# Kernel tuning notes

Hardware: AMD Instinct MI355X
Metric: run time of the kernel (lower is better)

Reference implementation:

```python
import jax, jax.numpy as jnp
import numpy as np
import math

IN_C, OUT_C, NUM_PARAM, STRIDE = 128, 256, 9, 1
BN_EPS = 1e-5


def _make_p_n(num_param):
    base_int = round(math.sqrt(num_param))
    row_number = num_param // base_int
    mod_number = num_param % base_int
    gx, gy = np.meshgrid(np.arange(row_number), np.arange(base_int), indexing='ij')
    px, py = gx.flatten(), gy.flatten()
    if mod_number > 0:
        mx, my = np.meshgrid(np.arange(row_number, row_number + 1), np.arange(mod_number), indexing='ij')
        px = np.concatenate([px, mx.flatten()])
        py = np.concatenate([py, my.flatten()])
    return np.concatenate([px, py]).astype(np.float32)  # (2N,)


def setup_inputs() -> dict:
    key = jax.random.key(0)
    ks = jax.random.split(key, 8)
    x = jax.random.normal(ks[0], (8, IN_C, 80, 80), dtype=jnp.float32)
    # offset-predicting conv (torch inits this to 0; use small random weights to exercise gathers)
    w_pconv = jax.random.normal(ks[1], (2 * NUM_PARAM, IN_C, 3, 3), dtype=jnp.float32) * 0.01
    b_pconv = jax.random.normal(ks[2], (2 * NUM_PARAM,), dtype=jnp.float32) * 0.1
    # final Conv: kernel (num_param, 1), stride (num_param, 1), pad 0, no bias
    w_conv = jax.random.normal(ks[3], (OUT_C, IN_C, NUM_PARAM, 1), dtype=jnp.float32) * (1.0 / math.sqrt(IN_C * NUM_PARAM))
    bn_gamma = jnp.ones((OUT_C,), jnp.float32) + 0.1 * jax.random.normal(ks[4], (OUT_C,), jnp.float32)
    bn_beta = 0.1 * jax.random.normal(ks[5], (OUT_C,), jnp.float32)
    bn_mean = 0.1 * jax.random.normal(ks[6], (OUT_C,), jnp.float32)
    bn_var = jnp.abs(jax.random.normal(ks[7], (OUT_C,), jnp.float32)) + 0.5
    p_n = jnp.asarray(_make_p_n(NUM_PARAM))
    return {"x": x, "w_pconv": w_pconv, "b_pconv": b_pconv, "w_conv": w_conv,
            "bn_gamma": bn_gamma, "bn_beta": bn_beta, "bn_mean": bn_mean,
            "bn_var": bn_var, "p_n": p_n}


def _conv2d(x, w, strides, padding):
    return jax.lax.conv_general_dilated(x, w, window_strides=strides, padding=padding,
                                        dimension_numbers=('NCHW', 'OIHW', 'NCHW'))


def reference(x, w_pconv, b_pconv, w_conv, bn_gamma, bn_beta, bn_mean, bn_var, p_n):
    b, c, H, W = x.shape
    # per-pixel offsets: [b, 2N, h, w]
    offset = _conv2d(x, w_pconv, (STRIDE, STRIDE), 'SAME') + b_pconv[None, :, None, None]
    N = offset.shape[1] // 2
    h, w = offset.shape[2], offset.shape[3]

    # sampling locations p = p_0 + p_n + offset
    px0 = jnp.broadcast_to((jnp.arange(h, dtype=x.dtype) * STRIDE)[None, None, :, None], (1, N, h, w))
    py0 = jnp.broadcast_to((jnp.arange(w, dtype=x.dtype) * STRIDE)[None, None, None, :], (1, N, h, w))
    p0 = jnp.concatenate([px0, py0], axis=1)  # [1, 2N, h, w]
    p = (p0 + p_n[None, :, None, None] + offset).transpose(0, 2, 3, 1)  # [b, h, w, 2N]

    def clamp2(t):
        return jnp.concatenate([jnp.clip(t[..., :N], 0, H - 1), jnp.clip(t[..., N:], 0, W - 1)], axis=-1)

    q_lt = clamp2(jnp.floor(p)).astype(jnp.int32)
    q_rb = clamp2(jnp.floor(p) + 1).astype(jnp.int32)
    q_lb = jnp.concatenate([q_lt[..., :N], q_rb[..., N:]], axis=-1)
    q_rt = jnp.concatenate([q_rb[..., :N], q_lt[..., N:]], axis=-1)
    pc = clamp2(p)

    # bilinear weights [b, h, w, N]
    def g(q, sx, sy):
        qf = q.astype(pc.dtype)
        return (1 + sx * (qf[..., :N] - pc[..., :N])) * (1 + sy * (qf[..., N:] - pc[..., N:]))

    g_lt, g_rb = g(q_lt, 1.0, 1.0), g(q_rb, -1.0, -1.0)
    g_lb, g_rt = g(q_lb, 1.0, -1.0), g(q_rt, -1.0, 1.0)

    x_flat = x.reshape(b, c, H * W)

    def gather(q):
        idx = (q[..., :N] * W + q[..., N:]).reshape(b, -1)  # [b, h*w*N]
        out = jax.vmap(lambda xf, i: xf[:, i])(x_flat, idx)  # [b, c, h*w*N]
        return out.reshape(b, c, h, w, N)

    x_off = (g_lt[:, None] * gather(q_lt) + g_rb[:, None] * gather(q_rb)
             + g_lb[:, None] * gather(q_lb) + g_rt[:, None] * gather(q_rt))

    # b c h w n -> b c (h n) w
    x_off = x_off.transpose(0, 1, 2, 4, 3).reshape(b, c, h * N, w)

    y = _conv2d(x_off, w_conv, (N, 1), 'VALID')  # [b, out_c, h, w]
    inv = jax.lax.rsqrt(bn_var + BN_EPS)
    y = (y - bn_mean[None, :, None, None]) * (bn_gamma * inv)[None, :, None, None] + bn_beta[None, :, None, None]
    return y * jax.nn.sigmoid(y)  # SiLU
```

## Files before the change

### kernel.cpp

```cpp
#include <hip/hip_runtime.h>
#include <hip/hip_bf16.h>


typedef __attribute__((ext_vector_type(8))) short bf16x8;
typedef __attribute__((ext_vector_type(4))) float f32x4;
typedef __attribute__((ext_vector_type(2))) float f32x2;
typedef __attribute__((ext_vector_type(4))) unsigned int u32x4;

#define NHW 6400
#define NPIX 80

__device__ __forceinline__ unsigned short f2bf(float f){
  __hip_bfloat16 h = __float2bfloat16(f);
  unsigned short u; __builtin_memcpy(&u, &h, 2); return u;
}
__device__ __forceinline__ f32x2 bfp2f(unsigned int u){
  union { unsigned int i; float f; } a, b;
  a.i = u << 16; b.i = u & 0xffff0000u;
  f32x2 r; r.x = a.f; r.y = b.f; return r;
}
__device__ __forceinline__ unsigned pk_bf16(float a, float b){
  unsigned r;
  asm("v_cvt_pk_bf16_f32 %0, %1, %2" : "=v"(r) : "v"(a), "v"(b));
  return r;
}
__device__ __forceinline__ void splitbf(float v, unsigned short& hi, unsigned short& lo){
  hi = f2bf(v);
  union { unsigned int i; float f; } h; h.i = (unsigned)hi << 16;
  lo = f2bf(v - h.f);
}
__device__ __forceinline__ float f16u2f(unsigned int u){
  unsigned short s = (unsigned short)u; _Float16 h;
  __builtin_memcpy(&h, &s, 2); return (float)h;
}
__device__ __forceinline__ unsigned short f2f16u(float f){
  _Float16 h = (_Float16)f; unsigned short s;
  __builtin_memcpy(&s, &h, 2); return s;
}
__device__ __forceinline__ float fast_silu(float v){
  float e, r;
  asm("v_exp_f32 %0, %1" : "=v"(e) : "v"(v * -1.44269504088896f));
  asm("v_rcp_f32 %0, %1" : "=v"(r) : "v"(1.0f + e));
  return v * r;
}

__global__ __launch_bounds__(256) void k_pre(const float* __restrict__ x,
                                             const float* __restrict__ w_conv,
                                             const float* __restrict__ w_pconv,
                                             const float* __restrict__ gamma,
                                             const float* __restrict__ beta,
                                             const float* __restrict__ mean,
                                             const float* __restrict__ var,
                                             unsigned short* __restrict__ xt,
                                             unsigned short* __restrict__ xtl,
                                             uint4* __restrict__ wf,
                                             uint4* __restrict__ wpfH,
                                             uint4* __restrict__ wpfL,
                                             float* __restrict__ shift){
  __shared__ unsigned short tileH[64 * 132];
  __shared__ unsigned short tileL[64 * 132];
  int blk = blockIdx.x; int t = threadIdx.x;
  if (blk < 800){
    int b = blk / 100; int pixbase = (blk % 100) * 64;
    int lane = t & 63; int cg = t >> 6;
    for (int ci = 0; ci < 32; ++ci){
      int c = cg * 32 + ci;
      float v = x[(b * 128 + c) * NHW + pixbase + lane];
      unsigned short hi, lo; splitbf(v, hi, lo);
      tileH[lane * 132 + c] = hi;
      tileL[lane * 132 + c] = lo;
    }
    __syncthreads();
    for (int i = 0; i < 8; ++i){
      int slot = t + i * 256; int m = slot >> 5; int c = (slot & 31) * 4;
      uint2 vH = *reinterpret_cast<const uint2*>(&tileH[m * 132 + c]);
      uint2 vL = *reinterpret_cast<const uint2*>(&tileL[m * 132 + c]);
      *reinterpret_cast<uint2*>(xt  + (b * NHW + pixbase + m) * 128 + c) = vH;
      *reinterpret_cast<uint2*>(xtl + (b * NHW + pixbase + m) * 128 + c) = vL;
    }
    return;
  }
  int pblk = blk - 800;
  if (pblk < 144){
    int id = pblk * 256 + t;
    int lane = id & 63, ofrag = (id >> 6) & 15, kc = (id >> 10) & 3, n = id >> 12;
    int o = ofrag * 16 + (lane & 15), cb = kc * 32 + ((lane >> 4) & 3) * 8;
    float sc = gamma[o] * rsqrtf(var[o] + 1e-5f);
    unsigned short h[8];
    for (int j = 0; j < 8; ++j) h[j] = f2bf(w_conv[(o * 128 + cb + j) * 9 + n] * sc);
    uint4 v;
    v.x = (unsigned)h[0] | ((unsigned)h[1] << 16);
    v.y = (unsigned)h[2] | ((unsigned)h[3] << 16);
    v.z = (unsigned)h[4] | ((unsigned)h[5] << 16);
    v.w = (unsigned)h[6] | ((unsigned)h[7] << 16);
    wf[id] = v;
  } else if (pblk < 180){
    int isLo = (pblk >= 162);
    int id = (pblk - (isLo ? 162 : 144)) * 256 + t;
    int lane = id & 63, ofrag = (id >> 6) & 1, kc = (id >> 7) & 3, tap = id >> 9;
    int o = ofrag * 16 + (lane & 15), cb = kc * 32 + ((lane >> 4) & 3) * 8;
    unsigned short h[8];
    for (int j = 0; j < 8; ++j){
      unsigned short hi = 0, lo = 0;
      if (o < 18) splitbf(w_pconv[(o * 128 + cb + j) * 9 + tap], hi, lo);
      h[j] = isLo ? lo : hi;
    }
    uint4 v;
    v.x = (unsigned)h[0] | ((unsigned)h[1] << 16);
    v.y = (unsigned)h[2] | ((unsigned)h[3] << 16);
    v.z = (unsigned)h[4] | ((unsigned)h[5] << 16);
    v.w = (unsigned)h[6] | ((unsigned)h[7] << 16);
    if (isLo) wpfL[id] = v; else wpfH[id] = v;
  } else {
    float sc = gamma[t] * rsqrtf(var[t] + 1e-5f);
    shift[t] = beta[t] - mean[t] * sc;
  }
}

__global__ __launch_bounds__(256, 6) void k_offconv(const unsigned short* __restrict__ xt,
                                                    const unsigned short* __restrict__ xtl,
                                                    const uint4* __restrict__ wpfH,
                                                    const uint4* __restrict__ wpfL,
                                                    const float* __restrict__ bpc,
                                                    const float* __restrict__ pn,
                                                    uint4* __restrict__ desc){
  int bid = blockIdx.x;
  int blk = (bid & 7) * 200 + (bid >> 3);
  int b = blk / 200; int pixbase = (blk % 200) * 32;
  int t = threadIdx.x; int lane = t & 63; int wv = t >> 6;
  int og = wv & 1;
  int pf = wv >> 1;
  __shared__ short BtileH[32 * 136];
  __shared__ short BtileL[32 * 136];
  __shared__ float off_lds[32 * 20];

  f32x4 acc = (f32x4){0.f, 0.f, 0.f, 0.f};
  const unsigned short* xbH = xt  + (size_t)b * NHW * 128;
  const unsigned short* xbL = xtl + (size_t)b * NHW * 128;

  int m_i[4], c_i[4], h_i[4], w_i[4];
#pragma unroll
  for (int i = 0; i < 4; ++i){
    int slot = t + i * 256;
    m_i[i] = slot >> 5; c_i[i] = (slot & 31) * 4;
    int p = pixbase + m_i[i];
    h_i[i] = p / NPIX; w_i[i] = p % NPIX;
  }

  uint2 rH[4], rL[4];

#define LOADTAP(DH, DW)                                                        \
  _Pragma("unroll")                                                            \
  for (int i = 0; i < 4; ++i){                                                 \
    int h2 = h_i[i] + (DH), w2 = w_i[i] + (DW);                                \
    uint2 vH; vH.x = 0u; vH.y = 0u;                                            \
    uint2 vL; vL.x = 0u; vL.y = 0u;                                            \
    if ((unsigned)h2 < NPIX && (unsigned)w2 < NPIX){                           \
      int off = (h2 * NPIX + w2) * 128 + c_i[i];                               \
      vH = *reinterpret_cast<const uint2*>(xbH + off);                         \
      vL = *reinterpret_cast<const uint2*>(xbL + off);                         \
    }                                                                          \
    rH[i] = vH; rL[i] = vL;                                                    \
  }

#define WRITETILE()                                                            \
  _Pragma("unroll")                                                            \
  for (int i = 0; i < 4; ++i){                                                 \
    *reinterpret_cast<uint2*>(&BtileH[m_i[i] * 136 + c_i[i]]) = rH[i];         \
    *reinterpret_cast<uint2*>(&BtileL[m_i[i] * 136 + c_i[i]]) = rL[i];         \
  }

  LOADTAP(-1, -1)
  WRITETILE()
  __syncthreads();

#pragma unroll 1
  for (int tap = 0; tap < 9; ++tap){
    if (tap < 8){
      int dh2 = (tap + 1) / 3 - 1, dw2 = (tap + 1) % 3 - 1;
      LOADTAP(dh2, dw2)
    }
#pragma unroll
    for (int kc = 0; kc < 4; ++kc){
      int boff = (pf * 16 + (lane & 15)) * 136 + kc * 32 + ((lane >> 4) & 3) * 8;
      bf16x8 bH = *reinterpret_cast<const bf16x8*>(&BtileH[boff]);
      bf16x8 bL = *reinterpret_cast<const bf16x8*>(&BtileL[boff]);
      int widx = ((tap * 4 + kc) * 2 + og) * 64 + lane;
      bf16x8 aH = *reinterpret_cast<const bf16x8*>(&wpfH[widx]);
      bf16x8 aL = *reinterpret_cast<const bf16x8*>(&wpfL[widx]);
      acc = __builtin_amdgcn_mfma_f32_16x16x32_bf16(aH, bH, acc, 0, 0, 0);
      acc = __builtin_amdgcn_mfma_f32_16x16x32_bf16(aH, bL, acc, 0, 0, 0);
      acc = __builtin_amdgcn_mfma_f32_16x16x32_bf16(aL, bH, acc, 0, 0, 0);
      acc = __builtin_amdgcn_mfma_f32_16x16x32_bf16(aL, bL, acc, 0, 0, 0);
    }
    __syncthreads();
    if (tap < 8){
      WRITETILE()
      __syncthreads();
    }
  }

  int pl = pf * 16 + (lane & 15);
#pragma unroll
  for (int r = 0; r < 4; ++r){
    int o = og * 16 + ((lane >> 4) & 3) * 4 + r;
    if (o < 18) off_lds[pl * 20 + o] = acc[r] + bpc[o];
  }
  __syncthreads();

  for (int item = t; item < 288; item += 256){
    int m = item / 9, n = item % 9;
    int p = pixbase + m; int h = p / NPIX, w = p % NPIX;
    float px = (float)h + pn[n]     + off_lds[m * 20 + n];
    float py = (float)w + pn[9 + n] + off_lds[m * 20 + 9 + n];
    float flx = floorf(px), fly = floorf(py);
    float qltx = fminf(fmaxf(flx, 0.f), 79.f);
    float qrbx = fminf(fmaxf(flx + 1.f, 0.f), 79.f);
    float qlty = fminf(fmaxf(fly, 0.f), 79.f);
    float qrby = fminf(fmaxf(fly + 1.f, 0.f), 79.f);
    float pcx = fminf(fmaxf(px, 0.f), 79.f);
    float pcy = fminf(fmaxf(py, 0.f), 79.f);
    float dxl = 1.f + (qltx - pcx), dxr = 1.f - (qrbx - pcx);
    float dyl = 1.f + (qlty - pcy), dyr = 1.f - (qrby - pcy);
    unsigned ix_l = (unsigned)(int)qltx, ix_r = (unsigned)(int)qrbx;
    unsigned iy_l = (unsigned)(int)qlty, iy_r = (unsigned)(int)qrby;
    uint4 d;
    d.x = (ix_l * NPIX + iy_l) | ((ix_r * NPIX + iy_r) << 16);
    d.y = (ix_l * NPIX + iy_r) | ((ix_r * NPIX + iy_l) << 16);
    d.z = (unsigned)f2f16u(dxl * dyl) | ((unsigned)f2f16u(dxr * dyr) << 16);
    d.w = (unsigned)f2f16u(dxl * dyr) | ((unsigned)f2f16u(dxr * dyl) << 16);
    desc[(size_t)(b * 9 + n) * NHW + p] = d;
  }
#undef LOADTAP
#undef WRITETILE
}

__global__ __launch_bounds__(256, 4) void k_main(const unsigned short* __restrict__ xt,
                                                 const uint4* __restrict__ desc,
                                                 const uint4* __restrict__ wf,
                                                 const float* __restrict__ shift,
                                                 float* __restrict__ out){
  int bid = blockIdx.x;
  int blk = (bid & 7) * 200 + (bid >> 3);
  int b = blk / 200; int pixbase = (blk % 200) * 32;
  int t = threadIdx.x; int lane = t & 63; int ow = t >> 6;
  __shared__ alignas(16) char A_lds[2][32 * 256];

  const char* xb = (const char*)(xt + (size_t)b * NHW * 128);
  const uint4* descb = desc + (size_t)b * 9 * NHW + pixbase;

  int m0 = t >> 4;
  int m1 = m0 + 16;
  int cb = (t & 15) * 16;
  int ls0 = m0 * 256 + (cb ^ ((m0 & 7) << 4));
  int ls1 = m1 * 256 + (cb ^ ((m1 & 7) << 4));

  f32x4 acc[4][2];
#pragma unroll
  for (int of = 0; of < 4; ++of)
#pragma unroll
    for (int pf = 0; pf < 2; ++pf)
      acc[of][pf] = (f32x4){0.f, 0.f, 0.f, 0.f};

  u32x4 GX[4], GY[4];
  uint2 zwX, zwY;
  uint4 dB0, dB1;

#define ISSUE_X()                                                              \
  {                                                                            \
    zwX.x = dB0.z; zwX.y = dB0.w;                                              \
    GX[0] = *reinterpret_cast<const u32x4*>(xb + (dB0.x & 0xffffu) * 256u + (unsigned)cb); \
    GX[1] = *reinterpret_cast<const u32x4*>(xb + (dB0.x >> 16)     * 256u + (unsigned)cb); \
    GX[2] = *reinterpret_cast<const u32x4*>(xb + (dB0.y & 0xffffu) * 256u + (unsigned)cb); \
    GX[3] = *reinterpret_cast<const u32x4*>(xb + (dB0.y >> 16)     * 256u + (unsigned)cb); \
  }

#define ISSUE_Y()                                                              \
  {                                                                            \
    zwY.x = dB1.z; zwY.y = dB1.w;                                              \
    GY[0] = *reinterpret_cast<const u32x4*>(xb + (dB1.x & 0xffffu) * 256u + (unsigned)cb); \
    GY[1] = *reinterpret_cast<const u32x4*>(xb + (dB1.x >> 16)     * 256u + (unsigned)cb); \
    GY[2] = *reinterpret_cast<const u32x4*>(xb + (dB1.y & 0xffffu) * 256u + (unsigned)cb); \
    GY[3] = *reinterpret_cast<const u32x4*>(xb + (dB1.y >> 16)     * 256u + (unsigned)cb); \
  }

#define COMB(G, ZW, LSO, WB)                                                   \
  {                                                                            \
    float w0 = f16u2f(ZW.x & 0xffffu), w1 = f16u2f(ZW.x >> 16);                \
    float w2 = f16u2f(ZW.y & 0xffffu), w3 = f16u2f(ZW.y >> 16);                \
    u32x4 pk;                                                                  \
    _Pragma("unroll")                                                          \
    for (int j = 0; j < 4; ++j){                                               \
      f32x2 a = w0 * bfp2f(G[0][j]) + w1 * bfp2f(G[1][j])                      \
              + w2 * bfp2f(G[2][j]) + w3 * bfp2f(G[3][j]);                     \
      pk[j] = pk_bf16(a.x, a.y);                                               \
    }                                                                          \
    *reinterpret_cast<u32x4*>((WB) + (LSO)) = pk;                              \
  }

#define MFMA_HALF(NN, KCA, KCB)                                                \
  {                                                                            \
    const char* ab = &A_lds[(NN) & 1][0];                                      \
    __builtin_amdgcn_s_setprio(1);                                             \
    _Pragma("unroll")                                                          \
    for (int kc = (KCA); kc <= (KCB); ++kc){                                   \
      bf16x8 bfrk[2];                                                          \
      _Pragma("unroll")                                                        \
      for (int pf = 0; pf < 2; ++pf){                                          \
        int row = pf * 16 + (lane & 15);                                       \
        bfrk[pf] = *reinterpret_cast<const bf16x8*>(                           \
            ab + row * 256 + ((kc * 64 + ((lane >> 4) & 3) * 16) ^ ((row & 7) << 4))); \
      }                                                                        \
      _Pragma("unroll")                                                        \
      for (int of = 0; of < 4; ++of){                                          \
        bf16x8 afr = *reinterpret_cast<const bf16x8*>(                         \
            &wf[((((NN) * 4 + kc) * 16) + ow * 4 + of) * 64 + lane]);          \
        _Pragma("unroll")                                                      \
        for (int pf = 0; pf < 2; ++pf)                                         \
          acc[of][pf] = __builtin_amdgcn_mfma_f32_16x16x32_bf16(afr, bfrk[pf], acc[of][pf], 0, 0, 0); \
      }                                                                        \
    }                                                                          \
    __builtin_amdgcn_s_setprio(0);                                             \
  }

#define STEP(NN)                                                               \
  {                                                                            \
    if ((NN) < 8){ ISSUE_X() }                                                 \
    if ((NN) < 7){ dB0 = descb[(size_t)((NN) + 2) * NHW + m0]; }               \
    MFMA_HALF(NN, 0, 1)                                                        \
    if ((NN) < 8){                                                             \
      COMB(GX, zwX, ls0, &A_lds[((NN) + 1) & 1][0])                            \
      __builtin_amdgcn_sched_barrier(0);                                       \
      ISSUE_Y()                                                                \
    }                                                                          \
    if ((NN) < 7){ dB1 = descb[(size_t)((NN) + 2) * NHW + m1]; }               \
    MFMA_HALF(NN, 2, 3)                                                        \
    if ((NN) < 8){                                                             \
      COMB(GY, zwY, ls1, &A_lds[((NN) + 1) & 1][0])                            \
    }                                                                          \
    __syncthreads();                                                           \
  }

  dB0 = descb[m0]; dB1 = descb[m1];
  ISSUE_X()
  COMB(GX, zwX, ls0, &A_lds[0][0])
  __builtin_amdgcn_sched_barrier(0);
  ISSUE_Y()
  COMB(GY, zwY, ls1, &A_lds[0][0])
  dB0 = descb[NHW + m0]; dB1 = descb[NHW + m1];
  __syncthreads();

  STEP(0) STEP(1) STEP(2) STEP(3) STEP(4) STEP(5) STEP(6) STEP(7) STEP(8)

#pragma unroll
  for (int of = 0; of < 4; ++of)
#pragma unroll
    for (int pf = 0; pf < 2; ++pf){
      int pix = pixbase + pf * 16 + (lane & 15);
#pragma unroll
      for (int r = 0; r < 4; ++r){
        int o = ow * 64 + of * 16 + ((lane >> 4) & 3) * 4 + r;
        float v = acc[of][pf][r] + shift[o];
        out[(size_t)(b * 256 + o) * NHW + pix] = fast_silu(v);
      }
    }
#undef ISSUE_X
#undef ISSUE_Y
#undef COMB
#undef MFMA_HALF
#undef STEP
}

extern "C" void kernel_launch(void* const* d_in, const int* in_sizes, int n_in,
                              void* d_out, int out_size, void* d_ws, size_t ws_size,
                              hipStream_t stream){
  const float* x       = (const float*)d_in[0];
  const float* w_pconv = (const float*)d_in[1];
  const float* b_pconv = (const float*)d_in[2];
  const float* w_conv  = (const float*)d_in[3];
  const float* gamma   = (const float*)d_in[4];
  const float* beta    = (const float*)d_in[5];
  const float* mean    = (const float*)d_in[6];
  const float* var     = (const float*)d_in[7];
  const float* pn      = (const float*)d_in[8];

  char* ws = (char*)d_ws;
  unsigned short* xt  = (unsigned short*)(ws + 0);
  unsigned short* xtl = (unsigned short*)(ws + 13107200);
  uint4* desc         = (uint4*)(ws + 26214400);
  uint4* wf           = (uint4*)(ws + 33587200);
  uint4* wpfH         = (uint4*)(ws + 34177024);
  uint4* wpfL         = (uint4*)(ws + 34250752);
  float* shift        = (float*)(ws + 34324480);
  float* out          = (float*)d_out;

  k_pre<<<981, 256, 0, stream>>>(x, w_conv, w_pconv, gamma, beta, mean, var,
                                 xt, xtl, wf, wpfH, wpfL, shift);
  k_offconv<<<1600, 256, 0, stream>>>(xt, xtl, wpfH, wpfL, b_pconv, pn, desc);
  k_main<<<1600, 256, 0, stream>>>(xt, desc, wf, shift, out);
}
```

Baseline: 116.7 us.

## Prefetch MFMA weight fragments into registers one step ahead and reorder gather pipeline

Weight fragments for the MFMA were loaded from global memory inline inside the MFMA loop. They are now prefetched into register arrays (Wa, Wb) during the previous step, so the MFMA loop reads only registers. The gather issue, combine and descriptor loads are reordered with sched_barriers: the X gathers are issued before the first MFMA half and combined after it, and the Y gathers follow the same pattern around the second half. This is meant to hide global-load latency behind matrix work, at the cost of 16 extra bf16x8 registers per thread, which may reduce occupancy.

```diff
diff --git a/kernel.cpp b/kernel.cpp
--- a/kernel.cpp
+++ b/kernel.cpp
@@ -263,12 +263,11 @@
       acc[of][pf] = (f32x4){0.f, 0.f, 0.f, 0.f};
 
   u32x4 GX[4], GY[4];
-  uint2 zwX, zwY;
   uint4 dB0, dB1;
+  bf16x8 Wa[8], Wb[8];
 
 #define ISSUE_X()                                                              \
   {                                                                            \
-    zwX.x = dB0.z; zwX.y = dB0.w;                                              \
     GX[0] = *reinterpret_cast<const u32x4*>(xb + (dB0.x & 0xffffu) * 256u + (unsigned)cb); \
     GX[1] = *reinterpret_cast<const u32x4*>(xb + (dB0.x >> 16)     * 256u + (unsigned)cb); \
     GX[2] = *reinterpret_cast<const u32x4*>(xb + (dB0.y & 0xffffu) * 256u + (unsigned)cb); \
@@ -277,17 +276,16 @@
 
 #define ISSUE_Y()                                                              \
   {                                                                            \
-    zwY.x = dB1.z; zwY.y = dB1.w;                                              \
     GY[0] = *reinterpret_cast<const u32x4*>(xb + (dB1.x & 0xffffu) * 256u + (unsigned)cb); \
     GY[1] = *reinterpret_cast<const u32x4*>(xb + (dB1.x >> 16)     * 256u + (unsigned)cb); \
     GY[2] = *reinterpret_cast<const u32x4*>(xb + (dB1.y & 0xffffu) * 256u + (unsigned)cb); \
     GY[3] = *reinterpret_cast<const u32x4*>(xb + (dB1.y >> 16)     * 256u + (unsigned)cb); \
   }
 
-#define COMB(G, ZW, LSO, WB)                                                   \
-  {                                                                            \
-    float w0 = f16u2f(ZW.x & 0xffffu), w1 = f16u2f(ZW.x >> 16);                \
-    float w2 = f16u2f(ZW.y & 0xffffu), w3 = f16u2f(ZW.y >> 16);                \
+#define COMB(G, D, LSO, WB)                                                    \
+  {                                                                            \
+    float w0 = f16u2f(D.z & 0xffffu), w1 = f16u2f(D.z >> 16);                  \
+    float w2 = f16u2f(D.w & 0xffffu), w3 = f16u2f(D.w >> 16);                  \
     u32x4 pk;                                                                  \
     _Pragma("unroll")                                                          \
     for (int j = 0; j < 4; ++j){                                               \
@@ -298,7 +296,17 @@
     *reinterpret_cast<u32x4*>((WB) + (LSO)) = pk;                              \
   }
 
-#define MFMA_HALF(NN, KCA, KCB)                                                \
+#define WLOAD(W, NN, KCA)                                                      \
+  {                                                                            \
+    _Pragma("unroll")                                                          \
+    for (int j = 0; j < 8; ++j){                                               \
+      int kc = (KCA) + (j >> 2); int of = j & 3;                               \
+      W[j] = *reinterpret_cast<const bf16x8*>(                                 \
+          &wf[((((NN) * 4 + kc) * 16) + ow * 4 + of) * 64 + lane]);            \
+    }                                                                          \
+  }
+
+#define MFMA_HALF(NN, KCA, KCB, W)                                             \
   {                                                                            \
     const char* ab = &A_lds[(NN) & 1][0];                                      \
     __builtin_amdgcn_s_setprio(1);                                             \
@@ -313,8 +321,7 @@
       }                                                                        \
       _Pragma("unroll")                                                        \
       for (int of = 0; of < 4; ++of){                                          \
-        bf16x8 afr = *reinterpret_cast<const bf16x8*>(                         \
-            &wf[((((NN) * 4 + kc) * 16) + ow * 4 + of) * 64 + lane]);          \
+        bf16x8 afr = W[(kc - (KCA)) * 4 + of];                                 \
         _Pragma("unroll")                                                      \
         for (int pf = 0; pf < 2; ++pf)                                         \
           acc[of][pf] = __builtin_amdgcn_mfma_f32_16x16x32_bf16(afr, bfrk[pf], acc[of][pf], 0, 0, 0); \
@@ -326,28 +333,37 @@
 #define STEP(NN)                                                               \
   {                                                                            \
     if ((NN) < 8){ ISSUE_X() }                                                 \
+    __builtin_amdgcn_sched_barrier(0);                                         \
+    MFMA_HALF(NN, 0, 1, Wa)                                                    \
+    if ((NN) < 8){                                                             \
+      WLOAD(Wa, (NN) + 1, 0)                                                   \
+      __builtin_amdgcn_sched_barrier(0);                                       \
+      COMB(GX, dB0, ls0, &A_lds[((NN) + 1) & 1][0])                            \
+    }                                                                          \
     if ((NN) < 7){ dB0 = descb[(size_t)((NN) + 2) * NHW + m0]; }               \
-    MFMA_HALF(NN, 0, 1)                                                        \
+    __builtin_amdgcn_sched_barrier(0);                                         \
+    if ((NN) < 8){ ISSUE_Y() }                                                 \
+    __builtin_amdgcn_sched_barrier(0);                                         \
+    MFMA_HALF(NN, 2, 3, Wb)                                                    \
     if ((NN) < 8){                                                             \
-      COMB(GX, zwX, ls0, &A_lds[((NN) + 1) & 1][0])                            \
+      WLOAD(Wb, (NN) + 1, 2)                                                   \
       __builtin_amdgcn_sched_barrier(0);                                       \
-      ISSUE_Y()                                                                \
+      COMB(GY, dB1, ls1, &A_lds[((NN) + 1) & 1][0])                            \
     }                                                                          \
     if ((NN) < 7){ dB1 = descb[(size_t)((NN) + 2) * NHW + m1]; }               \
-    MFMA_HALF(NN, 2, 3)                                                        \
-    if ((NN) < 8){                                                             \
-      COMB(GY, zwY, ls1, &A_lds[((NN) + 1) & 1][0])                            \
-    }                                                                          \
     __syncthreads();                                                           \
   }
 
   dB0 = descb[m0]; dB1 = descb[m1];
   ISSUE_X()
-  COMB(GX, zwX, ls0, &A_lds[0][0])
+  WLOAD(Wa, 0, 0)
+  WLOAD(Wb, 0, 2)
+  COMB(GX, dB0, ls0, &A_lds[0][0])
+  dB0 = descb[NHW + m0];
   __builtin_amdgcn_sched_barrier(0);
   ISSUE_Y()
-  COMB(GY, zwY, ls1, &A_lds[0][0])
-  dB0 = descb[NHW + m0]; dB1 = descb[NHW + m1];
+  COMB(GY, dB1, ls1, &A_lds[0][0])
+  dB1 = descb[NHW + m1];
   __syncthreads();
 
   STEP(0) STEP(1) STEP(2) STEP(3) STEP(4) STEP(5) STEP(6) STEP(7) STEP(8)
@@ -367,6 +383,7 @@
 #undef ISSUE_X
 #undef ISSUE_Y
 #undef COMB
+#undef WLOAD
 #undef MFMA_HALF
 #undef STEP
 }
```

Measured after the change: 167.4 us. 1.43x slower.

## Fuse offset conv and deformable gather-GEMM into one kernel via LDS descriptors

Applied to the files above, without the earlier changes.

Merges the offset-predicting conv kernel and the main gather/GEMM kernel into a single kernel with the same block-to-pixel mapping. Per-block sampling descriptors now stay in shared memory instead of a global round trip, which also removes one launch. Shared memory is aliased between the offset-conv tiles and the main A buffers. The cost is lower occupancy for the offset-conv phase (launch bounds 4 instead of 6) and serialisation of both phases within each block.

```diff
diff --git a/kernel.cpp b/kernel.cpp
--- a/kernel.cpp
+++ b/kernel.cpp
@@ -117,37 +117,42 @@
   }
 }
 
-__global__ __launch_bounds__(256, 6) void k_offconv(const unsigned short* __restrict__ xt,
-                                                    const unsigned short* __restrict__ xtl,
-                                                    const uint4* __restrict__ wpfH,
-                                                    const uint4* __restrict__ wpfL,
-                                                    const float* __restrict__ bpc,
-                                                    const float* __restrict__ pn,
-                                                    uint4* __restrict__ desc){
+__global__ __launch_bounds__(256, 4) void k_fused(const unsigned short* __restrict__ xt,
+                                                  const unsigned short* __restrict__ xtl,
+                                                  const uint4* __restrict__ wpfH,
+                                                  const uint4* __restrict__ wpfL,
+                                                  const float* __restrict__ bpc,
+                                                  const float* __restrict__ pn,
+                                                  const uint4* __restrict__ wf,
+                                                  const float* __restrict__ shift,
+                                                  float* __restrict__ out){
   int bid = blockIdx.x;
   int blk = (bid & 7) * 200 + (bid >> 3);
   int b = blk / 200; int pixbase = (blk % 200) * 32;
-  int t = threadIdx.x; int lane = t & 63; int wv = t >> 6;
-  int og = wv & 1;
-  int pf = wv >> 1;
-  __shared__ short BtileH[32 * 136];
-  __shared__ short BtileL[32 * 136];
-  __shared__ float off_lds[32 * 20];
-
-  f32x4 acc = (f32x4){0.f, 0.f, 0.f, 0.f};
-  const unsigned short* xbH = xt  + (size_t)b * NHW * 128;
-  const unsigned short* xbL = xtl + (size_t)b * NHW * 128;
-
-  int m_i[4], c_i[4], h_i[4], w_i[4];
-#pragma unroll
-  for (int i = 0; i < 4; ++i){
-    int slot = t + i * 256;
-    m_i[i] = slot >> 5; c_i[i] = (slot & 31) * 4;
-    int p = pixbase + m_i[i];
-    h_i[i] = p / NPIX; w_i[i] = p % NPIX;
-  }
-
-  uint2 rH[4], rL[4];
+  int t = threadIdx.x; int lane = t & 63;
+
+  __shared__ alignas(16) char smem[24576];
+  short* BtileH  = (short*)(smem);
+  short* BtileL  = (short*)(smem + 8704);
+  float* off_lds = (float*)(smem + 17408);
+  uint4* descL   = (uint4*)(smem + 19968);
+
+  {
+    int wv = t >> 6; int og = wv & 1; int pf = wv >> 1;
+    f32x4 acc = (f32x4){0.f, 0.f, 0.f, 0.f};
+    const unsigned short* xbH = xt  + (size_t)b * NHW * 128;
+    const unsigned short* xbL = xtl + (size_t)b * NHW * 128;
+
+    int m_i[4], c_i[4], h_i[4], w_i[4];
+#pragma unroll
+    for (int i = 0; i < 4; ++i){
+      int slot = t + i * 256;
+      m_i[i] = slot >> 5; c_i[i] = (slot & 31) * 4;
+      int p = pixbase + m_i[i];
+      h_i[i] = p / NPIX; w_i[i] = p % NPIX;
+    }
+
+    uint2 rH[4], rL[4];
 
 #define LOADTAP(DH, DW)                                                        \
   _Pragma("unroll")                                                            \
@@ -170,101 +175,96 @@
     *reinterpret_cast<uint2*>(&BtileL[m_i[i] * 136 + c_i[i]]) = rL[i];         \
   }
 
-  LOADTAP(-1, -1)
-  WRITETILE()
-  __syncthreads();
+    LOADTAP(-1, -1)
+    WRITETILE()
+    __syncthreads();
 
 #pragma unroll 1
-  for (int tap = 0; tap < 9; ++tap){
-    if (tap < 8){
-      int dh2 = (tap + 1) / 3 - 1, dw2 = (tap + 1) % 3 - 1;
-      LOADTAP(dh2, dw2)
-    }
-#pragma unroll
-    for (int kc = 0; kc < 4; ++kc){
-      int boff = (pf * 16 + (lane & 15)) * 136 + kc * 32 + ((lane >> 4) & 3) * 8;
-      bf16x8 bH = *reinterpret_cast<const bf16x8*>(&BtileH[boff]);
-      bf16x8 bL = *reinterpret_cast<const bf16x8*>(&BtileL[boff]);
-      int widx = ((tap * 4 + kc) * 2 + og) * 64 + lane;
-      bf16x8 aH = *reinterpret_cast<const bf16x8*>(&wpfH[widx]);
-      bf16x8 aL = *reinterpret_cast<const bf16x8*>(&wpfL[widx]);
-      acc = __builtin_amdgcn_mfma_f32_16x16x32_bf16(aH, bH, acc, 0, 0, 0);
-      acc = __builtin_amdgcn_mfma_f32_16x16x32_bf16(aH, bL, acc, 0, 0, 0);
-      acc = __builtin_amdgcn_mfma_f32_16x16x32_bf16(aL, bH, acc, 0, 0, 0);
-      acc = __builtin_amdgcn_mfma_f32_16x16x32_bf16(aL, bL, acc, 0, 0, 0);
+    for (int tap = 0; tap < 9; ++tap){
+      if (tap < 8){
+        int dh2 = (tap + 1) / 3 - 1, dw2 = (tap + 1) % 3 - 1;
+        LOADTAP(dh2, dw2)
+      }
+#pragma unroll
+      for (int kc = 0; kc < 4; ++kc){
+        int boff = (pf * 16 + (lane & 15)) * 136 + kc * 32 + ((lane >> 4) & 3) * 8;
+        bf16x8 bH = *reinterpret_cast<const bf16x8*>(&BtileH[boff]);
+        bf16x8 bL = *reinterpret_cast<const bf16x8*>(&BtileL[boff]);
+        int widx = ((tap * 4 + kc) * 2 + og) * 64 + lane;
+        bf16x8 aH = *reinterpret_cast<const bf16x8*>(&wpfH[widx]);
+        bf16x8 aL = *reinterpret_cast<const bf16x8*>(&wpfL[widx]);
+        acc = __builtin_amdgcn_mfma_f32_16x16x32_bf16(aH, bH, acc, 0, 0, 0);
+        acc = __builtin_amdgcn_mfma_f32_16x16x32_bf16(aH, bL, acc, 0, 0, 0);
+        acc = __builtin_amdgcn_mfma_f32_16x16x32_bf16(aL, bH, acc, 0, 0, 0);
+        acc = __builtin_amdgcn_mfma_f32_16x16x32_bf16(aL, bL, acc, 0, 0, 0);
+      }
+      __syncthreads();
+      if (tap < 8){
+        WRITETILE()
+        __syncthreads();
+      }
+    }
+
+    int pl = pf * 16 + (lane & 15);
+#pragma unroll
+    for (int r = 0; r < 4; ++r){
+      int o = og * 16 + ((lane >> 4) & 3) * 4 + r;
+      if (o < 18) off_lds[pl * 20 + o] = acc[r] + bpc[o];
     }
     __syncthreads();
-    if (tap < 8){
-      WRITETILE()
-      __syncthreads();
-    }
-  }
-
-  int pl = pf * 16 + (lane & 15);
-#pragma unroll
-  for (int r = 0; r < 4; ++r){
-    int o = og * 16 + ((lane >> 4) & 3) * 4 + r;
-    if (o < 18) off_lds[pl * 20 + o] = acc[r] + bpc[o];
-  }
-  __syncthreads();
-
-  for (int item = t; item < 288; item += 256){
-    int m = item / 9, n = item % 9;
-    int p = pixbase + m; int h = p / NPIX, w = p % NPIX;
-    float px = (float)h + pn[n]     + off_lds[m * 20 + n];
-    float py = (float)w + pn[9 + n] + off_lds[m * 20 + 9 + n];
-    float flx = floorf(px), fly = floorf(py);
-    float qltx = fminf(fmaxf(flx, 0.f), 79.f);
-    float qrbx = fminf(fmaxf(flx + 1.f, 0.f), 79.f);
-    float qlty = fminf(fmaxf(fly, 0.f), 79.f);
-    float qrby = fminf(fmaxf(fly + 1.f, 0.f), 79.f);
-    float pcx = fminf(fmaxf(px, 0.f), 79.f);
-    float pcy = fminf(fmaxf(py, 0.f), 79.f);
-    float dxl = 1.f + (qltx - pcx), dxr = 1.f - (qrbx - pcx);
-    float dyl = 1.f + (qlty - pcy), dyr = 1.f - (qrby - pcy);
-    unsigned ix_l = (unsigned)(int)qltx, ix_r = (unsigned)(int)qrbx;
-    unsigned iy_l = (unsigned)(int)qlty, iy_r = (unsigned)(int)qrby;
-    uint4 d;
-    d.x = (ix_l * NPIX + iy_l) | ((ix_r * NPIX + iy_r) << 16);
-    d.y = (ix_l * NPIX + iy_r) | ((ix_r * NPIX + iy_l) << 16);
-    d.z = (unsigned)f2f16u(dxl * dyl) | ((unsigned)f2f16u(dxr * dyr) << 16);
-    d.w = (unsigned)f2f16u(dxl * dyr) | ((unsigned)f2f16u(dxr * dyl) << 16);
-    desc[(size_t)(b * 9 + n) * NHW + p] = d;
-  }
+
+    for (int item = t; item < 288; item += 256){
+      int m = item / 9, n = item % 9;
+      int p = pixbase + m; int h = p / NPIX, w = p % NPIX;
+      float px = (float)h + pn[n]     + off_lds[m * 20 + n];
+      float py = (float)w + pn[9 + n] + off_lds[m * 20 + 9 + n];
+      float flx = floorf(px), fly = floorf(py);
+      float qltx = fminf(fmaxf(flx, 0.f), 79.f);
+      float qrbx = fminf(fmaxf(flx + 1.f, 0.f), 79.f);
+      float qlty = fminf(fmaxf(fly, 0.f), 79.f);
+      float qrby = fminf(fmaxf(fly + 1.f, 0.f), 79.f);
+      float pcx = fminf(fmaxf(px, 0.f), 79.f);
+      float pcy = fminf(fmaxf(py, 0.f), 79.f);
+      float dxl = 1.f + (qltx - pcx), dxr = 1.f - (qrbx - pcx);
+      float dyl = 1.f + (qlty - pcy), dyr = 1.f - (qrby - pcy);
+      unsigned ix_l = (unsigned)(int)qltx, ix_r = (unsigned)(int)qrbx;
+      unsigned iy_l = (unsigned)(int)qlty, iy_r = (unsigned)(int)qrby;
+      uint4 d;
+      d.x = (ix_l * NPIX + iy_l) | ((ix_r * NPIX + iy_r) << 16);
+      d.y = (ix_l * NPIX + iy_r) | ((ix_r * NPIX + iy_l) << 16);
+      d.z = (unsigned)f2f16u(dxl * dyl) | ((unsigned)f2f16u(dxr * dyr) << 16);
+      d.w = (unsigned)f2f16u(dxl * dyr) | ((unsigned)f2f16u(dxr * dyl) << 16);
+      descL[n * 32 + m] = d;
+    }
 #undef LOADTAP
 #undef WRITETILE
-}
-
-__global__ __launch_bounds__(256, 4) void k_main(const unsigned short* __restrict__ xt,
-                                                 const uint4* __restrict__ desc,
-                                                 const uint4* __restrict__ wf,
-                                                 const float* __restrict__ shift,
-                                                 float* __restrict__ out){
-  int bid = blockIdx.x;
-  int blk = (bid & 7) * 200 + (bid >> 3);
-  int b = blk / 200; int pixbase = (blk % 200) * 32;
-  int t = threadIdx.x; int lane = t & 63; int ow = t >> 6;
-  __shared__ alignas(16) char A_lds[2][32 * 256];
-
-  const char* xb = (const char*)(xt + (size_t)b * NHW * 128);
-  const uint4* descb = desc + (size_t)b * 9 * NHW + pixbase;
-
-  int m0 = t >> 4;
-  int m1 = m0 + 16;
-  int cb = (t & 15) * 16;
-  int ls0 = m0 * 256 + (cb ^ ((m0 & 7) << 4));
-  int ls1 = m1 * 256 + (cb ^ ((m1 & 7) << 4));
-
-  f32x4 acc[4][2];
-#pragma unroll
-  for (int of = 0; of < 4; ++of)
-#pragma unroll
-    for (int pf = 0; pf < 2; ++pf)
-      acc[of][pf] = (f32x4){0.f, 0.f, 0.f, 0.f};
-
-  u32x4 GX[4], GY[4];
-  uint2 zwX, zwY;
-  uint4 dB0, dB1;
+  }
+  __syncthreads();
+  __builtin_amdgcn_sched_barrier(0);
+
+  {
+    int ow = t >> 6;
+    char* A_lds0 = smem;
+    const char* xb = (const char*)(xt + (size_t)b * NHW * 128);
+
+    int m0 = t >> 4;
+    int m1 = m0 + 16;
+    int cb = (t & 15) * 16;
+    int ls0 = m0 * 256 + (cb ^ ((m0 & 7) << 4));
+    int ls1 = m1 * 256 + (cb ^ ((m1 & 7) << 4));
+
+    f32x4 acc[4][2];
+#pragma unroll
+    for (int of = 0; of < 4; ++of)
+#pragma unroll
+      for (int pf = 0; pf < 2; ++pf)
+        acc[of][pf] = (f32x4){0.f, 0.f, 0.f, 0.f};
+
+    u32x4 GX[4], GY[4];
+    uint2 zwX, zwY;
+    uint4 dB0, dB1;
+
+#define DLD(N, M) descL[(N) * 32 + (M)]
 
 #define ISSUE_X()                                                              \
   {                                                                            \
@@ -300,7 +300,7 @@
 
 #define MFMA_HALF(NN, KCA, KCB)                                                \
   {                                                                            \
-    const char* ab = &A_lds[(NN) & 1][0];                                      \
+    const char* ab = A_lds0 + ((NN) & 1) * 8192;                               \
     __builtin_amdgcn_s_setprio(1);                                             \
     _Pragma("unroll")                                                          \
     for (int kc = (KCA); kc <= (KCB); ++kc){                                   \
@@ -326,49 +326,51 @@
 #define STEP(NN)                                                               \
   {                                                                            \
     if ((NN) < 8){ ISSUE_X() }                                                 \
-    if ((NN) < 7){ dB0 = descb[(size_t)((NN) + 2) * NHW + m0]; }               \
+    if ((NN) < 7){ dB0 = DLD((NN) + 2, m0); }                                  \
     MFMA_HALF(NN, 0, 1)                                                        \
     if ((NN) < 8){                                                             \
-      COMB(GX, zwX, ls0, &A_lds[((NN) + 1) & 1][0])                            \
+      COMB(GX, zwX, ls0, A_lds0 + (((NN) + 1) & 1) * 8192)                     \
       __builtin_amdgcn_sched_barrier(0);                                       \
       ISSUE_Y()                                                                \
     }                                                                          \
-    if ((NN) < 7){ dB1 = descb[(size_t)((NN) + 2) * NHW + m1]; }               \
+    if ((NN) < 7){ dB1 = DLD((NN) + 2, m1); }                                  \
     MFMA_HALF(NN, 2, 3)                                                        \
     if ((NN) < 8){                                                             \
-      COMB(GY, zwY, ls1, &A_lds[((NN) + 1) & 1][0])                            \
+      COMB(GY, zwY, ls1, A_lds0 + (((NN) + 1) & 1) * 8192)                     \
     }                                                                          \
     __syncthreads();                                                           \
   }
 
-  dB0 = descb[m0]; dB1 = descb[m1];
-  ISSUE_X()
-  COMB(GX, zwX, ls0, &A_lds[0][0])
-  __builtin_amdgcn_sched_barrier(0);
-  ISSUE_Y()
-  COMB(GY, zwY, ls1, &A_lds[0][0])
-  dB0 = descb[NHW + m0]; dB1 = descb[NHW + m1];
-  __syncthreads();
-
-  STEP(0) STEP(1) STEP(2) STEP(3) STEP(4) STEP(5) STEP(6) STEP(7) STEP(8)
-
-#pragma unroll
-  for (int of = 0; of < 4; ++of)
-#pragma unroll
-    for (int pf = 0; pf < 2; ++pf){
-      int pix = pixbase + pf * 16 + (lane & 15);
-#pragma unroll
-      for (int r = 0; r < 4; ++r){
-        int o = ow * 64 + of * 16 + ((lane >> 4) & 3) * 4 + r;
-        float v = acc[of][pf][r] + shift[o];
-        out[(size_t)(b * 256 + o) * NHW + pix] = fast_silu(v);
+    dB0 = DLD(0, m0); dB1 = DLD(0, m1);
+    ISSUE_X()
+    COMB(GX, zwX, ls0, A_lds0)
+    __builtin_amdgcn_sched_barrier(0);
+    ISSUE_Y()
+    COMB(GY, zwY, ls1, A_lds0)
+    dB0 = DLD(1, m0); dB1 = DLD(1, m1);
+    __syncthreads();
+
+    STEP(0) STEP(1) STEP(2) STEP(3) STEP(4) STEP(5) STEP(6) STEP(7) STEP(8)
+
+#pragma unroll
+    for (int of = 0; of < 4; ++of)
+#pragma unroll
+      for (int pf = 0; pf < 2; ++pf){
+        int pix = pixbase + pf * 16 + (lane & 15);
+#pragma unroll
+        for (int r = 0; r < 4; ++r){
+          int o = ow * 64 + of * 16 + ((lane >> 4) & 3) * 4 + r;
+          float v = acc[of][pf][r] + shift[o];
+          out[(size_t)(b * 256 + o) * NHW + pix] = fast_silu(v);
+        }
       }
-    }
+#undef DLD
 #undef ISSUE_X
 #undef ISSUE_Y
 #undef COMB
 #undef MFMA_HALF
 #undef STEP
+  }
 }
 
 extern "C" void kernel_launch(void* const* d_in, const int* in_sizes, int n_in,
@@ -387,7 +389,6 @@
   char* ws = (char*)d_ws;
   unsigned short* xt  = (unsigned short*)(ws + 0);
   unsigned short* xtl = (unsigned short*)(ws + 13107200);
-  uint4* desc         = (uint4*)(ws + 26214400);
   uint4* wf           = (uint4*)(ws + 33587200);
   uint4* wpfH         = (uint4*)(ws + 34177024);
   uint4* wpfL         = (uint4*)(ws + 34250752);
@@ -396,6 +397,5 @@
 
   k_pre<<<981, 256, 0, stream>>>(x, w_conv, w_pconv, gamma, beta, mean, var,
                                  xt, xtl, wf, wpfH, wpfL, shift);
-  k_offconv<<<1600, 256, 0, stream>>>(xt, xtl, wpfH, wpfL, b_pconv, pn, desc);
-  k_main<<<1600, 256, 0, stream>>>(xt, desc, wf, shift, out);
-}
+  k_fused<<<1600, 256, 0, stream>>>(xt, xtl, wpfH, wpfL, b_pconv, pn, wf, shift, out);
+}
```

New measurement: 114.7 us, median of 2. Within noise of the previous version (-1.7%).

## Double pixel tile of main deformable GEMM kernel to 64 pixels per block

Applied to the files above, without the earlier changes.

The main kernel now processes 64 output pixels per block instead of 32, halving the grid to 800 blocks. Each weight fragment loaded from global memory is reused across four pixel fragments instead of two, which cuts weight traffic per MFMA. The gather/combine pipeline is split into four quarter slots interleaved with MFMA quarters. The price is more accumulator registers and twice the LDS per block, with launch bounds lowered to 3 blocks per SM, so occupancy and latency hiding drop.

```diff
diff --git a/kernel.cpp b/kernel.cpp
--- a/kernel.cpp
+++ b/kernel.cpp
@@ -235,59 +235,49 @@
 #undef WRITETILE
 }
 
-__global__ __launch_bounds__(256, 4) void k_main(const unsigned short* __restrict__ xt,
-                                                 const uint4* __restrict__ desc,
-                                                 const uint4* __restrict__ wf,
-                                                 const float* __restrict__ shift,
-                                                 float* __restrict__ out){
+__global__ __launch_bounds__(256, 3) void k_main64(const unsigned short* __restrict__ xt,
+                                                   const uint4* __restrict__ desc,
+                                                   const uint4* __restrict__ wf,
+                                                   const float* __restrict__ shift,
+                                                   float* __restrict__ out){
   int bid = blockIdx.x;
-  int blk = (bid & 7) * 200 + (bid >> 3);
-  int b = blk / 200; int pixbase = (blk % 200) * 32;
+  int blk = (bid & 7) * 100 + (bid >> 3);
+  int b = blk / 100; int pixbase = (blk % 100) * 64;
   int t = threadIdx.x; int lane = t & 63; int ow = t >> 6;
-  __shared__ alignas(16) char A_lds[2][32 * 256];
+  __shared__ alignas(16) char A_lds[2][64 * 256];
 
   const char* xb = (const char*)(xt + (size_t)b * NHW * 128);
   const uint4* descb = desc + (size_t)b * 9 * NHW + pixbase;
 
-  int m0 = t >> 4;
-  int m1 = m0 + 16;
+  int mrow = t >> 4;
   int cb = (t & 15) * 16;
-  int ls0 = m0 * 256 + (cb ^ ((m0 & 7) << 4));
-  int ls1 = m1 * 256 + (cb ^ ((m1 & 7) << 4));
-
-  f32x4 acc[4][2];
+  int lsw = cb ^ ((mrow & 7) << 4);
+
+#define M(S)  (mrow + (S) * 16)
+#define LS(S) ((mrow + (S) * 16) * 256 + lsw)
+
+  f32x4 acc[4][4];
 #pragma unroll
   for (int of = 0; of < 4; ++of)
 #pragma unroll
-    for (int pf = 0; pf < 2; ++pf)
+    for (int pf = 0; pf < 4; ++pf)
       acc[of][pf] = (f32x4){0.f, 0.f, 0.f, 0.f};
 
-  u32x4 GX[4], GY[4];
-  uint2 zwX, zwY;
-  uint4 dB0, dB1;
-
-#define ISSUE_X()                                                              \
-  {                                                                            \
-    zwX.x = dB0.z; zwX.y = dB0.w;                                              \
-    GX[0] = *reinterpret_cast<const u32x4*>(xb + (dB0.x & 0xffffu) * 256u + (unsigned)cb); \
-    GX[1] = *reinterpret_cast<const u32x4*>(xb + (dB0.x >> 16)     * 256u + (unsigned)cb); \
-    GX[2] = *reinterpret_cast<const u32x4*>(xb + (dB0.y & 0xffffu) * 256u + (unsigned)cb); \
-    GX[3] = *reinterpret_cast<const u32x4*>(xb + (dB0.y >> 16)     * 256u + (unsigned)cb); \
-  }
-
-#define ISSUE_Y()                                                              \
-  {                                                                            \
-    zwY.x = dB1.z; zwY.y = dB1.w;                                              \
-    GY[0] = *reinterpret_cast<const u32x4*>(xb + (dB1.x & 0xffffu) * 256u + (unsigned)cb); \
-    GY[1] = *reinterpret_cast<const u32x4*>(xb + (dB1.x >> 16)     * 256u + (unsigned)cb); \
-    GY[2] = *reinterpret_cast<const u32x4*>(xb + (dB1.y & 0xffffu) * 256u + (unsigned)cb); \
-    GY[3] = *reinterpret_cast<const u32x4*>(xb + (dB1.y >> 16)     * 256u + (unsigned)cb); \
-  }
-
-#define COMB(G, ZW, LSO, WB)                                                   \
-  {                                                                            \
-    float w0 = f16u2f(ZW.x & 0xffffu), w1 = f16u2f(ZW.x >> 16);                \
-    float w2 = f16u2f(ZW.y & 0xffffu), w3 = f16u2f(ZW.y >> 16);                \
+  u32x4 G[4];
+  uint4 dB0, dB1, dB2, dB3;
+
+#define ISSUE(D)                                                               \
+  {                                                                            \
+    G[0] = *reinterpret_cast<const u32x4*>(xb + (D.x & 0xffffu) * 256u + (unsigned)cb); \
+    G[1] = *reinterpret_cast<const u32x4*>(xb + (D.x >> 16)     * 256u + (unsigned)cb); \
+    G[2] = *reinterpret_cast<const u32x4*>(xb + (D.y & 0xffffu) * 256u + (unsigned)cb); \
+    G[3] = *reinterpret_cast<const u32x4*>(xb + (D.y >> 16)     * 256u + (unsigned)cb); \
+  }
+
+#define COMB(D, LSO, WB)                                                       \
+  {                                                                            \
+    float w0 = f16u2f(D.z & 0xffffu), w1 = f16u2f(D.z >> 16);                  \
+    float w2 = f16u2f(D.w & 0xffffu), w3 = f16u2f(D.w >> 16);                  \
     u32x4 pk;                                                                  \
     _Pragma("unroll")                                                          \
     for (int j = 0; j < 4; ++j){                                               \
@@ -298,56 +288,56 @@
     *reinterpret_cast<u32x4*>((WB) + (LSO)) = pk;                              \
   }
 
-#define MFMA_HALF(NN, KCA, KCB)                                                \
+#define MFMA_Q(NN, KC)                                                         \
   {                                                                            \
     const char* ab = &A_lds[(NN) & 1][0];                                      \
     __builtin_amdgcn_s_setprio(1);                                             \
+    bf16x8 bfrk[4];                                                            \
     _Pragma("unroll")                                                          \
-    for (int kc = (KCA); kc <= (KCB); ++kc){                                   \
-      bf16x8 bfrk[2];                                                          \
+    for (int pf = 0; pf < 4; ++pf){                                            \
+      int row = pf * 16 + (lane & 15);                                         \
+      bfrk[pf] = *reinterpret_cast<const bf16x8*>(                             \
+          ab + row * 256 + (((KC) * 64 + ((lane >> 4) & 3) * 16) ^ ((row & 7) << 4))); \
+    }                                                                          \
+    _Pragma("unroll")                                                          \
+    for (int of = 0; of < 4; ++of){                                            \
+      bf16x8 afr = *reinterpret_cast<const bf16x8*>(                           \
+          &wf[((((NN) * 4 + (KC)) * 16) + ow * 4 + of) * 64 + lane]);          \
       _Pragma("unroll")                                                        \
-      for (int pf = 0; pf < 2; ++pf){                                          \
-        int row = pf * 16 + (lane & 15);                                       \
-        bfrk[pf] = *reinterpret_cast<const bf16x8*>(                           \
-            ab + row * 256 + ((kc * 64 + ((lane >> 4) & 3) * 16) ^ ((row & 7) << 4))); \
-      }                                                                        \
-      _Pragma("unroll")                                                        \
-      for (int of = 0; of < 4; ++of){                                          \
-        bf16x8 afr = *reinterpret_cast<const bf16x8*>(                         \
-            &wf[((((NN) * 4 + kc) * 16) + ow * 4 + of) * 64 + lane]);          \
-        _Pragma("unroll")                                                      \
-        for (int pf = 0; pf < 2; ++pf)                                         \
-          acc[of][pf] = __builtin_amdgcn_mfma_f32_16x16x32_bf16(afr, bfrk[pf], acc[of][pf], 0, 0, 0); \
-      }                                                                        \
+      for (int pf = 0; pf < 4; ++pf)                                           \
+        acc[of][pf] = __builtin_amdgcn_mfma_f32_16x16x32_bf16(afr, bfrk[pf], acc[of][pf], 0, 0, 0); \
     }                                                                          \
     __builtin_amdgcn_s_setprio(0);                                             \
   }
 
+#define QSLOT(NN, S, DB)                                                       \
+  {                                                                            \
+    if ((NN) < 8){ ISSUE(DB) }                                                 \
+    MFMA_Q(NN, S)                                                              \
+    if ((NN) < 8){ COMB(DB, LS(S), &A_lds[((NN) + 1) & 1][0]) }                \
+    if ((NN) < 7){ DB = descb[(size_t)((NN) + 2) * NHW + M(S)]; }              \
+    __builtin_amdgcn_sched_barrier(0);                                         \
+  }
+
 #define STEP(NN)                                                               \
   {                                                                            \
-    if ((NN) < 8){ ISSUE_X() }                                                 \
-    if ((NN) < 7){ dB0 = descb[(size_t)((NN) + 2) * NHW + m0]; }               \
-    MFMA_HALF(NN, 0, 1)                                                        \
-    if ((NN) < 8){                                                             \
-      COMB(GX, zwX, ls0, &A_lds[((NN) + 1) & 1][0])                            \
-      __builtin_amdgcn_sched_barrier(0);                                       \
-      ISSUE_Y()                                                                \
-    }                                                                          \
-    if ((NN) < 7){ dB1 = descb[(size_t)((NN) + 2) * NHW + m1]; }               \
-    MFMA_HALF(NN, 2, 3)                                                        \
-    if ((NN) < 8){                                                             \
-      COMB(GY, zwY, ls1, &A_lds[((NN) + 1) & 1][0])                            \
-    }                                                                          \
+    QSLOT(NN, 0, dB0)                                                          \
+    QSLOT(NN, 1, dB1)                                                          \
+    QSLOT(NN, 2, dB2)                                                          \
+    QSLOT(NN, 3, dB3)                                                          \
     __syncthreads();                                                           \
   }
 
-  dB0 = descb[m0]; dB1 = descb[m1];
-  ISSUE_X()
-  COMB(GX, zwX, ls0, &A_lds[0][0])
+  dB0 = descb[M(0)]; dB1 = descb[M(1)]; dB2 = descb[M(2)]; dB3 = descb[M(3)];
+  ISSUE(dB0) COMB(dB0, LS(0), &A_lds[0][0])
   __builtin_amdgcn_sched_barrier(0);
-  ISSUE_Y()
-  COMB(GY, zwY, ls1, &A_lds[0][0])
-  dB0 = descb[NHW + m0]; dB1 = descb[NHW + m1];
+  ISSUE(dB1) COMB(dB1, LS(1), &A_lds[0][0])
+  __builtin_amdgcn_sched_barrier(0);
+  ISSUE(dB2) COMB(dB2, LS(2), &A_lds[0][0])
+  __builtin_amdgcn_sched_barrier(0);
+  ISSUE(dB3) COMB(dB3, LS(3), &A_lds[0][0])
+  dB0 = descb[NHW + M(0)]; dB1 = descb[NHW + M(1)];
+  dB2 = descb[NHW + M(2)]; dB3 = descb[NHW + M(3)];
   __syncthreads();
 
   STEP(0) STEP(1) STEP(2) STEP(3) STEP(4) STEP(5) STEP(6) STEP(7) STEP(8)
@@ -355,7 +345,7 @@
 #pragma unroll
   for (int of = 0; of < 4; ++of)
 #pragma unroll
-    for (int pf = 0; pf < 2; ++pf){
+    for (int pf = 0; pf < 4; ++pf){
       int pix = pixbase + pf * 16 + (lane & 15);
 #pragma unroll
       for (int r = 0; r < 4; ++r){
@@ -364,10 +354,12 @@
         out[(size_t)(b * 256 + o) * NHW + pix] = fast_silu(v);
       }
     }
-#undef ISSUE_X
-#undef ISSUE_Y
+#undef M
+#undef LS
+#undef ISSUE
 #undef COMB
-#undef MFMA_HALF
+#undef MFMA_Q
+#undef QSLOT
 #undef STEP
 }
 
@@ -397,5 +389,5 @@
   k_pre<<<981, 256, 0, stream>>>(x, w_conv, w_pconv, gamma, beta, mean, var,
                                  xt, xtl, wf, wpfH, wpfL, shift);
   k_offconv<<<1600, 256, 0, stream>>>(xt, xtl, wpfH, wpfL, b_pconv, pn, desc);
-  k_main<<<1600, 256, 0, stream>>>(xt, desc, wf, shift, out);
-}
+  k_main64<<<800, 256, 0, stream>>>(xt, desc, wf, shift, out);
+}
```

After: 128.9 us. 1.1x slower.
